# Performance work log

Measured on AMD Instinct MI355X. Metric: run time of the kernel, lower is better.

The kernel has to match this reference:

```python
import jax, jax.numpy as jnp
import numpy as np

WS = (7, 7)   # window size
SS = (3, 3)   # shift size
NH = 8        # num heads
DIM = 256
B_, H_, W_ = 16, 112, 112


def _rel_index(wh, ww):
    ch, cw = np.meshgrid(np.arange(wh), np.arange(ww), indexing='ij')
    cf = np.stack([ch, cw]).reshape(2, -1)
    rc = (cf[:, :, None] - cf[:, None, :]).transpose(1, 2, 0)
    rc[:, :, 0] += wh - 1
    rc[:, :, 1] += ww - 1
    rc[:, :, 0] *= 2 * ww - 1
    return rc.sum(-1).reshape(-1)


def _shift_mask(pH, pW, wh, ww, sh, sw):
    m = np.zeros((pH, pW))
    cnt = 0
    for h0, h1 in ((0, pH - wh), (pH - wh, pH - sh), (pH - sh, pH)):
        for w0, w1 in ((0, pW - ww), (pW - ww, pW - sw), (pW - sw, pW)):
            m[h0:h1, w0:w1] = cnt
            cnt += 1
    m = m.reshape(pH // wh, wh, pW // ww, ww).transpose(0, 2, 1, 3).reshape(-1, wh * ww)
    d = m[:, None, :] - m[:, :, None]  # (nW, N, N), [w,i,j] = m[w,j]-m[w,i]
    return np.where(d != 0, -100.0, 0.0).astype(np.float32)


def _partition(x, wh, ww):
    B, H, W, C = x.shape
    x = x.reshape(B, H // wh, wh, W // ww, ww, C).transpose(0, 1, 3, 2, 4, 5)
    return x.reshape(B * (H // wh) * (W // ww), wh * ww, C)


def _unpartition(x, B, H, W, wh, ww):
    C = x.shape[-1]
    x = x.reshape(B, H // wh, W // ww, wh, ww, C).transpose(0, 1, 3, 2, 4, 5)
    return x.reshape(B, H, W, C)


def setup_inputs() -> dict:
    key = jax.random.key(0)
    ks = jax.random.split(key, 12)
    D = DIM
    inp = {
        'Q': jax.random.normal(ks[0], (B_, H_, W_, D), jnp.float32),
        'K': jax.random.normal(ks[1], (B_, H_, W_, D), jnp.float32),
        'V': jax.random.normal(ks[2], (B_, H_, W_, D), jnp.float32),
        'Qw': jax.random.normal(ks[3], (D, D), jnp.float32) * 0.02,
        'Qb': jax.random.normal(ks[4], (D,), jnp.float32) * 0.02,
        'Kw': jax.random.normal(ks[5], (D, D), jnp.float32) * 0.02,
        'Kb': jax.random.normal(ks[6], (D,), jnp.float32) * 0.02,
        'Vw': jax.random.normal(ks[7], (D, D), jnp.float32) * 0.02,
        'Vb': jax.random.normal(ks[8], (D,), jnp.float32) * 0.02,
        'Pw': jax.random.normal(ks[9], (D, D), jnp.float32) * 0.02,
        'Pb': jax.random.normal(ks[10], (D,), jnp.float32) * 0.02,
        'rpb_table': jax.random.normal(ks[11], ((2 * WS[0] - 1) * (2 * WS[1] - 1), NH), jnp.float32) * 0.02,
        'rp_index': jnp.asarray(_rel_index(WS[0], WS[1]), jnp.int32),
    }
    return inp


def reference(Q, K, V, Qw, Qb, Kw, Kb, Vw, Vb, Pw, Pb, rpb_table, rp_index):
    wh, ww = WS
    nh = NH
    B, H, W, C = Q.shape
    N = wh * ww
    hd = C // nh
    pad_b = (wh - H % wh) % wh
    pad_r = (ww - W % ww) % ww
    if pad_b or pad_r:
        pad = ((0, 0), (0, pad_b), (0, pad_r), (0, 0))
        Q, K, V = jnp.pad(Q, pad), jnp.pad(K, pad), jnp.pad(V, pad)
    pH, pW = H + pad_b, W + pad_r
    sh = 0 if wh >= pH else SS[0]
    sw = 0 if ww >= pW else SS[1]
    shifted = (sh + sw) > 0
    if shifted:
        Q = jnp.roll(Q, (-sh, -sw), (1, 2))
        K = jnp.roll(K, (-sh, -sw), (1, 2))
        V = jnp.roll(V, (-sh, -sw), (1, 2))
    xq = _partition(Q, wh, ww)  # (B*nW, N, C)
    xk = _partition(K, wh, ww)
    xv = _partition(V, wh, ww)
    q = (xq @ Qw.T + Qb).reshape(-1, N, nh, hd).transpose(0, 2, 1, 3) * (hd ** -0.5)
    k = (xk @ Kw.T + Kb).reshape(-1, N, nh, hd).transpose(0, 2, 1, 3)
    v = (xv @ Vw.T + Vb).reshape(-1, N, nh, hd).transpose(0, 2, 1, 3)
    bias = rpb_table[rp_index].reshape(N, N, nh).transpose(2, 0, 1)  # (nh, N, N)
    attn = jnp.einsum('bhnd,bhmd->bhnm', q, k) + bias[None]
    if shifted:
        mask = jnp.asarray(_shift_mask(pH, pW, wh, ww, sh, sw))  # (nW, N, N)
        nW = (pH // wh) * (pW // ww)
        attn = attn.reshape(B, nW, nh, N, N) + mask[None, :, None]
        attn = attn.reshape(-1, nh, N, N)
    attn = jax.nn.softmax(attn, axis=-1)
    x = jnp.einsum('bhnm,bhmd->bhnd', attn, v).transpose(0, 2, 1, 3).reshape(-1, N, C)
    x = x @ Pw.T + Pb
    x = _unpartition(x, B, pH, pW, wh, ww)
    if shifted:
        x = jnp.roll(x, (sh, sw), (1, 2))
    return x[:, :H, :W, :]
```

## Files before the change

### kernel.cpp

```cpp
#include <hip/hip_runtime.h>


typedef short  bf16x4_t __attribute__((ext_vector_type(4)));
typedef short  bf16x8_t __attribute__((ext_vector_type(8)));
typedef float  f32x4_t  __attribute__((ext_vector_type(4)));
typedef int    i32x4_t  __attribute__((ext_vector_type(4)));

#define HH    112
#define WWDIM 112
#define NTOK  49
#define NWIN  4096
#define SHIFT 3
#define LOG2E 1.4426950408889634f
#define MASKS (-144.26950408889634f)

__device__ __forceinline__ unsigned short f2bf(float f) {
  unsigned u = __builtin_bit_cast(unsigned, f);
  u += 0x7FFFu + ((u >> 16) & 1u);
  return (unsigned short)(u >> 16);
}

__device__ __forceinline__ unsigned cvtpk(float a, float b) {
  unsigned r;
  asm("v_cvt_pk_bf16_f32 %0, %1, %2" : "=v"(r) : "v"(a), "v"(b));
  return r;
}

__device__ __forceinline__ float exp2fast(float x) {
  float r;
  asm("v_exp_f32 %0, %1" : "=v"(r) : "v"(x));
  return r;
}

__device__ __forceinline__ bf16x8_t ld8(const unsigned short* p) {
  return __builtin_bit_cast(bf16x8_t, *reinterpret_cast<const i32x4_t*>(p));
}

__device__ __forceinline__ bf16x4_t pack4(float a, float b, float c, float d) {
  union { unsigned u[2]; bf16x4_t v; } t;
  t.u[0] = cvtpk(a, b); t.u[1] = cvtpk(c, d);
  return t.v;
}

__device__ __forceinline__ void gload16(const float* g, float* l) {
  __builtin_amdgcn_global_load_lds(
      (const __attribute__((address_space(1))) void*)g,
      (__attribute__((address_space(3))) void*)l, 16, 0, 0);
}

__device__ __forceinline__ bf16x8_t ldx(const float* Xf, int tok, int kk) {
  const int base = tok << 8;
  const int cs = (((kk >> 2) ^ (tok & 7)) << 2);
  const f32x4_t a = *reinterpret_cast<const f32x4_t*>(Xf + base + cs);
  const f32x4_t c = *reinterpret_cast<const f32x4_t*>(Xf + base + (cs ^ 4));
  union { unsigned u[4]; bf16x8_t v; } t;
  t.u[0] = cvtpk(a[0], a[1]); t.u[1] = cvtpk(a[2], a[3]);
  t.u[2] = cvtpk(c[0], c[1]); t.u[3] = cvtpk(c[2], c[3]);
  return t.v;
}

__device__ __forceinline__ int swzi(int row, int col, int rowElems) {
  int by = col << 1;
  int sb = (((by >> 4) ^ (row & 7)) << 4) | (by & 15);
  return row * rowElems + (sb >> 1);
}

__global__ void prep_kernel(const float* __restrict__ Qw, const float* __restrict__ Kw,
                            const float* __restrict__ Vw, const float* __restrict__ Pw,
                            const float* __restrict__ rpb, const int* __restrict__ rpi,
                            unsigned short* __restrict__ wbf, float* __restrict__ biasP) {
  int idx = blockIdx.x * 256 + threadIdx.x;
  if (idx < 4 * 65536) {
    int which = idx >> 16, e = idx & 65535;
    const float* s = (which == 0) ? Qw : (which == 1) ? Kw : (which == 2) ? Vw : Pw;
    wbf[idx] = f2bf(s[e]);
  }
  if (idx < 8 * 49 * 64) {
    int h = idx / 3136, r = idx - h * 3136;
    int i = r >> 6, j = r & 63;
    biasP[idx] = (i < NTOK && j < NTOK) ? rpb[rpi[i * NTOK + j] * 8 + h] * LOG2E : 0.f;
  }
}

#define GSTAGE(SRC)                                                           \
  do {                                                                        \
    _Pragma("unroll") for (int it = 0; it < 16; ++it) {                       \
      const int row = wid + (it << 2);                                        \
      gload16((SRC) + goff[it] + ((it & 1) ? (f0 ^ 16) : f0),                 \
              Xf + (row << 8));                                               \
    }                                                                         \
  } while (0)

#define WLOAD(WP, KS, S)                                                      \
  do {                                                                        \
    _Pragma("unroll") for (int m = 0; m < 4; ++m)                             \
      bwr[S][m] = ld8(&(WP)[(((wid << 6) + (m << 4) + lo) << 8) +             \
                            ((KS) << 5) + kof]);                              \
  } while (0)

__global__ __launch_bounds__(256, 2) void fused_kernel(
    const float* __restrict__ Qin, const float* __restrict__ Kin, const float* __restrict__ Vin,
    const float* __restrict__ Qbv, const float* __restrict__ Kbv, const float* __restrict__ Vbv,
    const float* __restrict__ Pbv,
    const unsigned short* __restrict__ wbf, const float* __restrict__ biasP,
    float* __restrict__ out) {
  __shared__ float Xf[64 * 256];
  unsigned short* Ab = (unsigned short*)Xf;

  const int blk = blockIdx.x, tid = threadIdx.x;
  const int lane = tid & 63, wid = tid >> 6;
  const int b = blk >> 8, wi = (blk >> 4) & 15, wj = blk & 15;
  const int lo = lane & 15, hi = lane >> 4;
  const int g4 = hi << 2, kof = hi << 3;
  const int f0 = (lane ^ wid) << 2;

  unsigned goff[16];
#pragma unroll
  for (int it = 0; it < 16; ++it) {
    int row = wid + (it << 2);
    unsigned off = 0;
    if (row < NTOK) {
      int i = row / 7, j = row - i * 7;
      int h_ = wi * 7 + i + SHIFT; if (h_ >= HH) h_ -= HH;
      int w_ = wj * 7 + j + SHIFT; if (w_ >= WWDIM) w_ -= WWDIM;
      off = ((unsigned)((b * HH + h_) * WWDIM + w_) << 8);
    }
    goff[it] = off;
  }

  bf16x8_t bwr[2][4];
  bf16x4_t qf[4][4], kf[4][4], vf[4][4];

  GSTAGE(Qin);
  __syncthreads();

#pragma unroll
  for (int ph = 0; ph < 2; ++ph) {
    const unsigned short* W_ = wbf + (ph << 16);
    f32x4_t acc[4][4];
#pragma unroll
    for (int a = 0; a < 4; ++a)
#pragma unroll
      for (int c = 0; c < 4; ++c) acc[a][c] = (f32x4_t){0.f, 0.f, 0.f, 0.f};
    WLOAD(W_, 0, 0);
#pragma unroll
    for (int ks = 0; ks < 8; ++ks) {
      if (ks < 7) WLOAD(W_, ks + 1, (ks + 1) & 1);
      const int kk = (ks << 5) + kof;
      bf16x8_t xb[4];
#pragma unroll
      for (int nj = 0; nj < 4; ++nj) xb[nj] = ldx(Xf, (nj << 4) + lo, kk);
#pragma unroll
      for (int m = 0; m < 4; ++m)
#pragma unroll
        for (int nj = 0; nj < 4; ++nj)
          acc[m][nj] = __builtin_amdgcn_mfma_f32_16x16x32_bf16(bwr[ks & 1][m], xb[nj], acc[m][nj], 0, 0, 0);
    }
    __syncthreads();
    GSTAGE(ph == 0 ? Kin : Vin);

    const float* bias = (ph == 0) ? Qbv : Kbv;
    const float scale = (ph == 0) ? 0.17677669529663687f * LOG2E : 1.0f;
#pragma unroll
    for (int m = 0; m < 4; ++m) {
      const float4 bb = *reinterpret_cast<const float4*>(bias + (wid << 6) + (m << 4) + g4);
#pragma unroll
      for (int nj = 0; nj < 4; ++nj) {
        const bf16x4_t v = pack4((acc[m][nj][0] + bb.x) * scale, (acc[m][nj][1] + bb.y) * scale,
                                 (acc[m][nj][2] + bb.z) * scale, (acc[m][nj][3] + bb.w) * scale);
        if (ph == 0) qf[m][nj] = v; else kf[m][nj] = v;
      }
    }
    __syncthreads();
  }

  {
    const unsigned short* W_ = wbf + (2 << 16);
    f32x4_t acc[4][4];
#pragma unroll
    for (int a = 0; a < 4; ++a)
#pragma unroll
      for (int c = 0; c < 4; ++c) acc[a][c] = (f32x4_t){0.f, 0.f, 0.f, 0.f};
    WLOAD(W_, 0, 0);
#pragma unroll
    for (int ks = 0; ks < 8; ++ks) {
      if (ks < 7) WLOAD(W_, ks + 1, (ks + 1) & 1);
      const int kk = (ks << 5) + kof;
      bf16x8_t xa[4];
#pragma unroll
      for (int mi = 0; mi < 4; ++mi) xa[mi] = ldx(Xf, (mi << 4) + lo, kk);
#pragma unroll
      for (int mi = 0; mi < 4; ++mi)
#pragma unroll
        for (int t = 0; t < 4; ++t)
          acc[mi][t] = __builtin_amdgcn_mfma_f32_16x16x32_bf16(xa[mi], bwr[ks & 1][t], acc[mi][t], 0, 0, 0);
    }
    __syncthreads();
    float bbv[4];
#pragma unroll
    for (int t = 0; t < 4; ++t) bbv[t] = Vbv[(wid << 6) + (t << 4) + lo];
#pragma unroll
    for (int mi = 0; mi < 4; ++mi)
#pragma unroll
      for (int t = 0; t < 4; ++t)
        vf[mi][t] = pack4(acc[mi][t][0] + bbv[t], acc[mi][t][1] + bbv[t],
                          acc[mi][t][2] + bbv[t], acc[mi][t][3] + bbv[t]);
  }

  const bool wi15 = (wi == 15), wj15 = (wj == 15);
  unsigned kbi = 0, kbj = 0, kval = 0;
#pragma unroll
  for (int njk = 0; njk < 4; ++njk)
#pragma unroll
    for (int rg = 0; rg < 4; ++rg) {
      int kt = (njk << 4) + g4 + rg;
      if (kt < NTOK) {
        int ti = kt / 7, tj = kt - (kt / 7) * 7;
        unsigned bit = 1u << (njk * 4 + rg);
        kval |= bit;
        if (ti >= 4) kbi |= bit;
        if (tj >= 4) kbj |= bit;
      }
    }

#pragma unroll
  for (int hh = 0; hh < 2; ++hh) {
    const int h = (wid << 1) + hh;
    const int co = h << 5;

    bf16x4_t pf[4][4];
#pragma unroll
    for (int njq = 0; njq < 4; ++njq) {
      const int qt = (njq << 4) + lo;
      const bool qv = qt < NTOK;
      const int sqt = qv ? qt : 0;
      const float* bq = biasP + h * 3136 + (sqt << 6);
      f32x4_t bfr[4];
#pragma unroll
      for (int njk = 0; njk < 4; ++njk)
        bfr[njk] = *reinterpret_cast<const f32x4_t*>(bq + (njk << 4) + g4);

      f32x4_t stc[4];
      __builtin_amdgcn_s_setprio(1);
#pragma unroll
      for (int njk = 0; njk < 4; ++njk) {
        stc[njk] = __builtin_amdgcn_mfma_f32_16x16x16bf16_1k(
            kf[(hh << 1)][njk], qf[(hh << 1)][njq], (f32x4_t){0.f, 0.f, 0.f, 0.f}, 0, 0, 0);
        stc[njk] = __builtin_amdgcn_mfma_f32_16x16x16bf16_1k(
            kf[(hh << 1) + 1][njk], qf[(hh << 1) + 1][njq], stc[njk], 0, 0, 0);
      }
      __builtin_amdgcn_s_setprio(0);

      const int qti = sqt / 7, qtj = sqt - (sqt / 7) * 7;
      const bool qbi = qti >= 4, qbj = qtj >= 4;
      float sum = 0.f;
#pragma unroll
      for (int njk = 0; njk < 4; ++njk)
#pragma unroll
        for (int rg = 0; rg < 4; ++rg) {
          const int bit = njk * 4 + rg;
          const bool valid = qv && ((kval >> bit) & 1u);
          float v = stc[njk][rg] + bfr[njk][rg];
          if (wi15 && (qbi != (bool)((kbi >> bit) & 1u))) v += MASKS;
          if (wj15 && (qbj != (bool)((kbj >> bit) & 1u))) v += MASKS;
          v = valid ? v : -1e30f;
          const float e = exp2fast(v);
          stc[njk][rg] = e;
          sum += e;
        }
      sum += __shfl_xor(sum, 16);
      sum += __shfl_xor(sum, 32);
      const float inv = __builtin_amdgcn_rcpf(sum);
#pragma unroll
      for (int njk = 0; njk < 4; ++njk)
        pf[njk][njq] = pack4(stc[njk][0] * inv, stc[njk][1] * inv,
                             stc[njk][2] * inv, stc[njk][3] * inv);
    }

    f32x4_t o[2][4];
#pragma unroll
    for (int a = 0; a < 2; ++a)
#pragma unroll
      for (int c = 0; c < 4; ++c) o[a][c] = (f32x4_t){0.f, 0.f, 0.f, 0.f};
    __builtin_amdgcn_s_setprio(1);
#pragma unroll
    for (int mi = 0; mi < 4; ++mi)
#pragma unroll
      for (int t2 = 0; t2 < 2; ++t2)
#pragma unroll
        for (int njq = 0; njq < 4; ++njq)
          o[t2][njq] = __builtin_amdgcn_mfma_f32_16x16x16bf16_1k(
              vf[mi][(hh << 1) + t2], pf[mi][njq], o[t2][njq], 0, 0, 0);
    __builtin_amdgcn_s_setprio(0);

#pragma unroll
    for (int t2 = 0; t2 < 2; ++t2)
#pragma unroll
      for (int njq = 0; njq < 4; ++njq) {
        const int qt = (njq << 4) + lo;
        const int ch0 = co + (t2 << 4) + g4;
        *reinterpret_cast<uint2*>(&Ab[swzi(qt, ch0, 256)]) =
            make_uint2(cvtpk(o[t2][njq][0], o[t2][njq][1]),
                       cvtpk(o[t2][njq][2], o[t2][njq][3]));
      }
  }
  __syncthreads();

  {
    const unsigned short* W_ = wbf + (3 << 16);
    f32x4_t y[4][4];
#pragma unroll
    for (int a = 0; a < 4; ++a)
#pragma unroll
      for (int c = 0; c < 4; ++c) y[a][c] = (f32x4_t){0.f, 0.f, 0.f, 0.f};
    WLOAD(W_, 0, 0);
#pragma unroll
    for (int ks = 0; ks < 8; ++ks) {
      if (ks < 7) WLOAD(W_, ks + 1, (ks + 1) & 1);
      const int kk = (ks << 5) + kof;
      bf16x8_t xb[4];
#pragma unroll
      for (int nj = 0; nj < 4; ++nj) xb[nj] = ld8(&Ab[swzi((nj << 4) + lo, kk, 256)]);
#pragma unroll
      for (int m = 0; m < 4; ++m)
#pragma unroll
        for (int nj = 0; nj < 4; ++nj)
          y[m][nj] = __builtin_amdgcn_mfma_f32_16x16x32_bf16(bwr[ks & 1][m], xb[nj], y[m][nj], 0, 0, 0);
    }
#pragma unroll
    for (int nj = 0; nj < 4; ++nj) {
      const int tok = (nj << 4) + lo;
      if (tok < NTOK) {
        const int i = tok / 7, j = tok - (tok / 7) * 7;
        int h_ = wi * 7 + i + SHIFT; if (h_ >= HH) h_ -= HH;
        int w_ = wj * 7 + j + SHIFT; if (w_ >= WWDIM) w_ -= WWDIM;
        float* ob = out + ((size_t)((b * HH + h_) * WWDIM + w_) << 8);
#pragma unroll
        for (int m = 0; m < 4; ++m) {
          const int ch0 = (wid << 6) + (m << 4) + g4;
          const float4 pb = *reinterpret_cast<const float4*>(Pbv + ch0);
          *reinterpret_cast<float4*>(ob + ch0) =
              make_float4(y[m][nj][0] + pb.x, y[m][nj][1] + pb.y,
                          y[m][nj][2] + pb.z, y[m][nj][3] + pb.w);
        }
      }
    }
  }
}

extern "C" void kernel_launch(void* const* d_in, const int* in_sizes, int n_in,
                              void* d_out, int out_size, void* d_ws, size_t ws_size,
                              hipStream_t stream) {
  const float* Q   = (const float*)d_in[0];
  const float* K   = (const float*)d_in[1];
  const float* V   = (const float*)d_in[2];
  const float* Qw  = (const float*)d_in[3];
  const float* Qb  = (const float*)d_in[4];
  const float* Kw  = (const float*)d_in[5];
  const float* Kb  = (const float*)d_in[6];
  const float* Vw  = (const float*)d_in[7];
  const float* Vb  = (const float*)d_in[8];
  const float* Pw  = (const float*)d_in[9];
  const float* Pb  = (const float*)d_in[10];
  const float* rpb = (const float*)d_in[11];
  const int*   rpi = (const int*)d_in[12];

  unsigned short* wbf = (unsigned short*)d_ws;
  float* biasP = (float*)(wbf + 4 * 65536);

  const size_t need = (size_t)4 * 65536 * 2 + (size_t)8 * 49 * 64 * 4;
  if (ws_size < need) return;

  prep_kernel<<<1024, 256, 0, stream>>>(Qw, Kw, Vw, Pw, rpb, rpi, wbf, biasP);
  fused_kernel<<<NWIN, 256, 0, stream>>>(Q, K, V, Qb, Kb, Vb, Pb, wbf, biasP,
                                         (float*)d_out);
}
```

Baseline: 407.3 us.

## Overlap V tile load with QK softmax and recompute gather offsets inline

Moves the V projection GEMM after the QK^T plus softmax computation for both heads. The global V staging issued at the end of the K phase can then land in shared memory while the softmax math runs, hiding load latency. Softmax probabilities for both heads are now held in registers (pfa/pfb) until after the V projection. The per-row gather offset array is removed and recomputed inline to save registers. Keeping both heads' probabilities live raises register pressure, which may cut occupancy or cause spills.

```diff
diff --git a/kernel.cpp b/kernel.cpp
--- a/kernel.cpp
+++ b/kernel.cpp
@@ -86,8 +86,14 @@
   do {                                                                        \
     _Pragma("unroll") for (int it = 0; it < 16; ++it) {                       \
       const int row = wid + (it << 2);                                        \
-      gload16((SRC) + goff[it] + ((it & 1) ? (f0 ^ 16) : f0),                 \
-              Xf + (row << 8));                                               \
+      unsigned off = 0;                                                       \
+      if (row < NTOK) {                                                       \
+        int i_ = row / 7, j_ = row - i_ * 7;                                  \
+        int h_ = wi * 7 + i_ + SHIFT; if (h_ >= HH) h_ -= HH;                 \
+        int w_ = wj * 7 + j_ + SHIFT; if (w_ >= WWDIM) w_ -= WWDIM;           \
+        off = ((unsigned)((b * HH + h_) * WWDIM + w_) << 8);                  \
+      }                                                                       \
+      gload16((SRC) + off + ((it & 1) ? (f0 ^ 16) : f0), Xf + (row << 8));    \
     }                                                                         \
   } while (0)
 
@@ -114,20 +120,6 @@
   const int g4 = hi << 2, kof = hi << 3;
   const int f0 = (lane ^ wid) << 2;
 
-  unsigned goff[16];
-#pragma unroll
-  for (int it = 0; it < 16; ++it) {
-    int row = wid + (it << 2);
-    unsigned off = 0;
-    if (row < NTOK) {
-      int i = row / 7, j = row - i * 7;
-      int h_ = wi * 7 + i + SHIFT; if (h_ >= HH) h_ -= HH;
-      int w_ = wj * 7 + j + SHIFT; if (w_ >= WWDIM) w_ -= WWDIM;
-      off = ((unsigned)((b * HH + h_) * WWDIM + w_) << 8);
-    }
-    goff[it] = off;
-  }
-
   bf16x8_t bwr[2][4];
   bf16x4_t qf[4][4], kf[4][4], vf[4][4];
 
@@ -171,40 +163,7 @@
         if (ph == 0) qf[m][nj] = v; else kf[m][nj] = v;
       }
     }
-    __syncthreads();
-  }
-
-  {
-    const unsigned short* W_ = wbf + (2 << 16);
-    f32x4_t acc[4][4];
-#pragma unroll
-    for (int a = 0; a < 4; ++a)
-#pragma unroll
-      for (int c = 0; c < 4; ++c) acc[a][c] = (f32x4_t){0.f, 0.f, 0.f, 0.f};
-    WLOAD(W_, 0, 0);
-#pragma unroll
-    for (int ks = 0; ks < 8; ++ks) {
-      if (ks < 7) WLOAD(W_, ks + 1, (ks + 1) & 1);
-      const int kk = (ks << 5) + kof;
-      bf16x8_t xa[4];
-#pragma unroll
-      for (int mi = 0; mi < 4; ++mi) xa[mi] = ldx(Xf, (mi << 4) + lo, kk);
-#pragma unroll
-      for (int mi = 0; mi < 4; ++mi)
-#pragma unroll
-        for (int t = 0; t < 4; ++t)
-          acc[mi][t] = __builtin_amdgcn_mfma_f32_16x16x32_bf16(xa[mi], bwr[ks & 1][t], acc[mi][t], 0, 0, 0);
-    }
-    __syncthreads();
-    float bbv[4];
-#pragma unroll
-    for (int t = 0; t < 4; ++t) bbv[t] = Vbv[(wid << 6) + (t << 4) + lo];
-#pragma unroll
-    for (int mi = 0; mi < 4; ++mi)
-#pragma unroll
-      for (int t = 0; t < 4; ++t)
-        vf[mi][t] = pack4(acc[mi][t][0] + bbv[t], acc[mi][t][1] + bbv[t],
-                          acc[mi][t][2] + bbv[t], acc[mi][t][3] + bbv[t]);
+    if (ph == 0) __syncthreads();
   }
 
   const bool wi15 = (wi == 15), wj15 = (wj == 15);
@@ -223,12 +182,10 @@
       }
     }
 
+  bf16x4_t pfa[4][4], pfb[4][4];
 #pragma unroll
   for (int hh = 0; hh < 2; ++hh) {
     const int h = (wid << 1) + hh;
-    const int co = h << 5;
-
-    bf16x4_t pf[4][4];
 #pragma unroll
     for (int njq = 0; njq < 4; ++njq) {
       const int qt = (njq << 4) + lo;
@@ -272,11 +229,52 @@
       sum += __shfl_xor(sum, 32);
       const float inv = __builtin_amdgcn_rcpf(sum);
 #pragma unroll
-      for (int njk = 0; njk < 4; ++njk)
-        pf[njk][njq] = pack4(stc[njk][0] * inv, stc[njk][1] * inv,
-                             stc[njk][2] * inv, stc[njk][3] * inv);
-    }
-
+      for (int njk = 0; njk < 4; ++njk) {
+        const bf16x4_t pv = pack4(stc[njk][0] * inv, stc[njk][1] * inv,
+                                  stc[njk][2] * inv, stc[njk][3] * inv);
+        if (hh == 0) pfa[njk][njq] = pv; else pfb[njk][njq] = pv;
+      }
+    }
+  }
+
+  WLOAD(wbf + (2 << 16), 0, 0);
+  __syncthreads();
+
+  {
+    const unsigned short* W_ = wbf + (2 << 16);
+    f32x4_t acc[4][4];
+#pragma unroll
+    for (int a = 0; a < 4; ++a)
+#pragma unroll
+      for (int c = 0; c < 4; ++c) acc[a][c] = (f32x4_t){0.f, 0.f, 0.f, 0.f};
+#pragma unroll
+    for (int ks = 0; ks < 8; ++ks) {
+      if (ks < 7) WLOAD(W_, ks + 1, (ks + 1) & 1);
+      const int kk = (ks << 5) + kof;
+      bf16x8_t xa[4];
+#pragma unroll
+      for (int mi = 0; mi < 4; ++mi) xa[mi] = ldx(Xf, (mi << 4) + lo, kk);
+#pragma unroll
+      for (int mi = 0; mi < 4; ++mi)
+#pragma unroll
+        for (int t = 0; t < 4; ++t)
+          acc[mi][t] = __builtin_amdgcn_mfma_f32_16x16x32_bf16(xa[mi], bwr[ks & 1][t], acc[mi][t], 0, 0, 0);
+    }
+    __syncthreads();
+    float bbv[4];
+#pragma unroll
+    for (int t = 0; t < 4; ++t) bbv[t] = Vbv[(wid << 6) + (t << 4) + lo];
+#pragma unroll
+    for (int mi = 0; mi < 4; ++mi)
+#pragma unroll
+      for (int t = 0; t < 4; ++t)
+        vf[mi][t] = pack4(acc[mi][t][0] + bbv[t], acc[mi][t][1] + bbv[t],
+                          acc[mi][t][2] + bbv[t], acc[mi][t][3] + bbv[t]);
+  }
+
+#pragma unroll
+  for (int hh = 0; hh < 2; ++hh) {
+    const int co = ((wid << 1) + hh) << 5;
     f32x4_t o[2][4];
 #pragma unroll
     for (int a = 0; a < 2; ++a)
@@ -290,7 +288,8 @@
 #pragma unroll
         for (int njq = 0; njq < 4; ++njq)
           o[t2][njq] = __builtin_amdgcn_mfma_f32_16x16x16bf16_1k(
-              vf[mi][(hh << 1) + t2], pf[mi][njq], o[t2][njq], 0, 0, 0);
+              vf[mi][(hh << 1) + t2],
+              (hh == 0) ? pfa[mi][njq] : pfb[mi][njq], o[t2][njq], 0, 0, 0);
     __builtin_amdgcn_s_setprio(0);
 
 #pragma unroll
```

Result: slower. 421.1 us (+3.4%).
